# Kernel tuning notes

Measured on AMD Instinct MI355X. Metric: run time of the kernel, lower is better.

## Reference

```python
import jax, jax.numpy as jnp
import numpy as np

NUM_HEAD = 8
EMBED_DIM = 512


def setup_inputs() -> dict:
    key = jax.random.key(0)
    ks = jax.random.split(key, 9)
    B, N, D = 4, 2048, 512
    # xavier_uniform bound for square [D, D] weights
    bound = float(np.sqrt(6.0 / (D + EMBED_DIM)))
    return {
        "q": jax.random.normal(ks[0], (B, N, D), jnp.float32),
        "k": jax.random.normal(ks[1], (B, N, D), jnp.float32),
        "v": jax.random.normal(ks[2], (B, N, D), jnp.float32),
        "Wq": jax.random.uniform(ks[3], (D, EMBED_DIM), jnp.float32, -bound, bound),
        "Wk": jax.random.uniform(ks[4], (D, EMBED_DIM), jnp.float32, -bound, bound),
        "Wv": jax.random.uniform(ks[5], (D, EMBED_DIM), jnp.float32, -bound, bound),
        "bq": jnp.zeros((EMBED_DIM,), jnp.float32),
        "bk": jnp.zeros((EMBED_DIM,), jnp.float32),
        "bv": jnp.zeros((EMBED_DIM,), jnp.float32),
    }


def reference(q, k, v, Wq, Wk, Wv, bq, bk, bv):
    h = NUM_HEAD
    ch = EMBED_DIM // h
    B, N, _ = q.shape
    # linear projections
    Q = q @ Wq + bq  # [B, N, E]
    K = k @ Wk + bk
    V = v @ Wv + bv
    # split heads: b n (h ch) -> b h n ch
    Q = Q.reshape(B, N, h, ch).transpose(0, 2, 1, 3)
    K = K.reshape(B, N, h, ch).transpose(0, 2, 1, 3)
    V = V.reshape(B, N, h, ch).transpose(0, 2, 1, 3)
    scale = 1.0 / np.sqrt(ch).astype(np.float32)
    scores = jnp.einsum("bhqc,bhkc->bhqk", Q, K) * scale  # [B, h, N, N]
    attn = jax.nn.softmax(scores, axis=-1)
    out = jnp.einsum("bhqk,bhkc->bhqc", attn, V)  # [B, h, N, ch]
    # merge heads: b h n ch -> b n (h ch)
    return out.transpose(0, 2, 1, 3).reshape(B, N, EMBED_DIM)
```

## Files before the change

### kernel.cpp

```cpp
#include <hip/hip_runtime.h>
#include <hip/hip_bf16.h>
#include <cstdint>

#define B_ 4
#define N_ 2048
#define D_ 512
#define E_ 512
#define H_ 8
#define CH_ 64
#define M_ (B_*N_)

typedef __attribute__((ext_vector_type(8))) short bf16x8;
typedef __attribute__((ext_vector_type(4))) float f32x4;
typedef __attribute__((ext_vector_type(16))) float f32x16;
using u16 = unsigned short;
using u32 = unsigned int;

__device__ __forceinline__ u16 f2bf(float f) {
  union { __hip_bfloat16 h; u16 u; } cv;
  cv.h = __float2bfloat16(f);
  return cv.u;
}

__device__ __forceinline__ float fexp2(float x) {
#if __has_builtin(__builtin_amdgcn_exp2f)
  return __builtin_amdgcn_exp2f(x);
#else
  return exp2f(x);
#endif
}

__device__ __forceinline__ void async16(const void* g, void* l) {
  __builtin_amdgcn_global_load_lds(
      (__attribute__((address_space(1))) void*)(g),
      (__attribute__((address_space(3))) void*)(l),
      16, 0, 0);
}

__global__ void prep(const float* __restrict__ q, const float* __restrict__ k,
                     const float* __restrict__ v,
                     const float* __restrict__ Wq, const float* __restrict__ Wk,
                     const float* __restrict__ Wv,
                     u16* __restrict__ qb, u16* __restrict__ kb, u16* __restrict__ vb,
                     u16* __restrict__ tq, u16* __restrict__ tk, u16* __restrict__ tv) {
  int bid = blockIdx.x;
  if (bid < 12288) {
    int t = bid >> 12;
    const float* in = (t == 0) ? q : (t == 1 ? k : v);
    u16* outp = (t == 0) ? qb : (t == 1 ? kb : vb);
    int i = ((bid & 4095) << 8) + threadIdx.x;
    float4 f = reinterpret_cast<const float4*>(in)[i];
    ushort4 o;
    o.x = f2bf(f.x); o.y = f2bf(f.y); o.z = f2bf(f.z); o.w = f2bf(f.w);
    reinterpret_cast<ushort4*>(outp)[i] = o;
  } else {
    bid -= 12288;
    int t = bid >> 10;
    const float* W = (t == 0) ? Wq : (t == 1 ? Wk : Wv);
    u16* T = (t == 0) ? tq : (t == 1 ? tk : tv);
    int idx = ((bid & 1023) << 8) + threadIdx.x;
    int e = idx >> 9, kd = idx & 511;
    T[idx] = f2bf(W[kd * E_ + e]);
  }
}

#define GBM 128
#define GBN 128
#define GBK 64

__global__ __launch_bounds__(256) void proj_gemm(
    const u16* __restrict__ xq, const u16* __restrict__ xk, const u16* __restrict__ xv,
    const u16* __restrict__ wtq, const u16* __restrict__ wtk, const u16* __restrict__ wtv,
    const float* __restrict__ bq, const float* __restrict__ bk, const float* __restrict__ bv,
    u16* __restrict__ Qp, u16* __restrict__ Kp, u16* __restrict__ Vp) {
  const int z = blockIdx.z;
  const u16* X  = (z == 0) ? xq : (z == 1 ? xk : xv);
  const u16* WT = (z == 0) ? wtq : (z == 1 ? wtk : wtv);
  const float* bias = (z == 0) ? bq : (z == 1 ? bk : bv);
  u16* Out = (z == 0) ? Qp : (z == 1 ? Kp : Vp);
  const float scale = (z == 0) ? 0.18033688011112042f : 1.0f;
  const bool vlayout = (z == 2);

  __shared__ __align__(16) u16 As[GBM * GBK];
  __shared__ __align__(16) u16 Bs[GBN * GBK];

  const int tid = threadIdx.x;
  const int l = tid & 63, w = tid >> 6;
  const int wr = w >> 1, wc = w & 1;
  const int m0 = blockIdx.y * GBM;
  const int e0 = blockIdx.x * GBN;

  f32x4 acc[4][4] = {};

  for (int ks = 0; ks < D_ / GBK; ++ks) {
    const int k0 = ks * GBK;
#pragma unroll
    for (int i = 0; i < 4; ++i) {
      int o = i * 4096 + tid * 16;
      int row = o >> 7, colb = o & 127;
      int scol = colb ^ ((row & 7) << 4);
      async16((const char*)X  + ((size_t)(m0 + row) * D_ + k0) * 2 + scol, (char*)As + o);
      async16((const char*)WT + ((size_t)(e0 + row) * D_ + k0) * 2 + scol, (char*)Bs + o);
    }
    __syncthreads();
#pragma unroll
    for (int kk = 0; kk < 2; ++kk) {
      bf16x8 af[4], bfr[4];
#pragma unroll
      for (int m = 0; m < 4; ++m) {
        int row = wr * 64 + m * 16 + (l & 15);
        int addr = (row << 7) + kk * 64 + ((l >> 4) << 4);
        addr ^= (row & 7) << 4;
        af[m] = *reinterpret_cast<const bf16x8*>((const char*)As + addr);
      }
#pragma unroll
      for (int n = 0; n < 4; ++n) {
        int row = wc * 64 + n * 16 + (l & 15);
        int addr = (row << 7) + kk * 64 + ((l >> 4) << 4);
        addr ^= (row & 7) << 4;
        bfr[n] = *reinterpret_cast<const bf16x8*>((const char*)Bs + addr);
      }
#pragma unroll
      for (int m = 0; m < 4; ++m)
#pragma unroll
        for (int n = 0; n < 4; ++n)
          acc[m][n] = __builtin_amdgcn_mfma_f32_16x16x32_bf16(af[m], bfr[n], acc[m][n], 0, 0, 0);
    }
    __syncthreads();
  }

#pragma unroll
  for (int m = 0; m < 4; ++m) {
#pragma unroll
    for (int n = 0; n < 4; ++n) {
      int ge = e0 + wc * 64 + n * 16 + (l & 15);
      int h = ge >> 6, c = ge & 63;
      float bv_ = bias[ge];
      int gm0 = m0 + wr * 64 + m * 16 + ((l >> 4) << 2);
      int b = gm0 >> 11, nn0 = gm0 & 2047;
      if (vlayout) {
        short4 sv;
#pragma unroll
        for (int j = 0; j < 4; ++j)
          ((u16*)&sv)[j] = f2bf((acc[m][n][j] + bv_) * scale);
        int np = (((nn0 >> 2) ^ (nn0 >> 3)) & 1) ? (nn0 ^ 12) : nn0;
        *reinterpret_cast<short4*>(
            &Out[(((size_t)b * H_ + h) * CH_ + c) * N_ + np]) = sv;
      } else {
#pragma unroll
        for (int j = 0; j < 4; ++j) {
          u16 oval = f2bf((acc[m][n][j] + bv_) * scale);
          Out[((((size_t)b * H_ + h) * N_ + nn0 + j) << 6) + c] = oval;
        }
      }
    }
  }
}

#define QBLK 128
#define KVB 64
#define NTH 16

#define MFMA32(A, Bv, C) __builtin_amdgcn_mfma_f32_32x32x16_bf16((A), (Bv), (C), 0, 0, 0)

__global__ __launch_bounds__(512, 2) void attn_kernel(
    const u16* __restrict__ Qp, const u16* __restrict__ Kp, const u16* __restrict__ Vp,
    float* __restrict__ out) {
  __shared__ __align__(16) u16 Kb[2][2][KVB * 64];
  __shared__ __align__(16) u16 Vb[2][2][KVB * 64];

  const int tid = threadIdx.x;
  const int l = tid & 63, w = tid >> 6;
  const int wsub = w & 3, hf = w >> 2;
  const int qcol = l & 31, hi = l >> 5;

  const int beta = blockIdx.x;
  const int xcd = beta & 7, r = beta >> 3;
  const int bh = xcd * 4 + (r >> 4);
  const int qt = r & 15;

  const u16* Qh = Qp + (size_t)bh * N_ * CH_;
  const u16* Kh = Kp + (size_t)bh * N_ * CH_;
  const u16* Vh = Vp + (size_t)bh * CH_ * N_;
  const int bb = bh >> 3, hh = bh & 7;
  const int qrow = qt * QBLK + wsub * 32 + qcol;

  bf16x8 qf[4];
  {
    const u16* qptr = Qh + (size_t)qrow * CH_;
#pragma unroll
    for (int ks = 0; ks < 4; ++ks)
      qf[ks] = *reinterpret_cast<const bf16x8*>(qptr + ks * 16 + hi * 8);
  }

  f32x16 o0 = {}, o1 = {};
  float lrun = 0.f;

  const int rowA = qcol << 7;
  const int swz  = (l & 7) << 4;
  const int hi16 = hi << 4;
  const int st   = tid & 255;
  const int tb   = hf * NTH;

#define STAGE(BUF, KV) do {                                                      \
    _Pragma("unroll")                                                            \
    for (int i = 0; i < 2; ++i) {                                                \
      int o = i * 4096 + st * 16;                                                \
      int row = o >> 7, colb = o & 127;                                          \
      int scol = colb ^ ((row & 7) << 4);                                        \
      async16((const char*)Kh + ((size_t)((KV) + row) << 7) + scol,              \
              (char*)&Kb[BUF][hf][0] + o);                                       \
      async16((const char*)Vh + ((size_t)row * N_ + (KV)) * 2 + scol,            \
              (char*)&Vb[BUF][hf][0] + o);                                       \
    } } while (0)

#define TILE(BUF, TL) do {                                                       \
    if ((TL) + 1 < NTH) STAGE((BUF) ^ 1, (tb + (TL) + 1) * KVB);                 \
    f32x16 s0 = {}, s1 = {};                                                     \
    __builtin_amdgcn_s_setprio(1);                                               \
    _Pragma("unroll")                                                            \
    for (int ks = 0; ks < 4; ++ks) {                                             \
      int col = (ks * 32 + hi16) ^ swz;                                          \
      bf16x8 k0 = *reinterpret_cast<const bf16x8*>((const char*)&Kb[BUF][hf][0] + rowA + col);        \
      bf16x8 k1 = *reinterpret_cast<const bf16x8*>((const char*)&Kb[BUF][hf][0] + 4096 + rowA + col); \
      s0 = MFMA32(k0, qf[ks], s0);                                               \
      s1 = MFMA32(k1, qf[ks], s1);                                               \
    }                                                                            \
    __builtin_amdgcn_s_setprio(0);                                               \
    _Pragma("unroll")                                                            \
    for (int rr = 0; rr < 16; ++rr) { s0[rr] = fexp2(s0[rr]); s1[rr] = fexp2(s1[rr]); } \
    {                                                                            \
      float t0 = (s0[0] + s0[1]) + (s0[2] + s0[3]);                              \
      float t1 = (s0[4] + s0[5]) + (s0[6] + s0[7]);                              \
      float t2 = (s0[8] + s0[9]) + (s0[10] + s0[11]);                            \
      float t3 = (s0[12] + s0[13]) + (s0[14] + s0[15]);                          \
      float t4 = (s1[0] + s1[1]) + (s1[2] + s1[3]);                              \
      float t5 = (s1[4] + s1[5]) + (s1[6] + s1[7]);                              \
      float t6 = (s1[8] + s1[9]) + (s1[10] + s1[11]);                            \
      float t7 = (s1[12] + s1[13]) + (s1[14] + s1[15]);                          \
      float rsum = ((t0 + t1) + (t2 + t3)) + ((t4 + t5) + (t6 + t7));            \
      rsum += __shfl_xor(rsum, 32);                                              \
      lrun += rsum;                                                              \
    }                                                                            \
    __builtin_amdgcn_s_setprio(1);                                               \
    _Pragma("unroll")                                                            \
    for (int ks = 0; ks < 4; ++ks) {                                             \
      const f32x16& sv = (ks < 2) ? s0 : s1;                                     \
      const int b0 = 8 * (ks & 1);                                               \
      union { u16 us[8]; bf16x8 v8; } pu;                                        \
      _Pragma("unroll")                                                          \
      for (int j = 0; j < 8; ++j) pu.us[j] = f2bf(sv[b0 + j]);                   \
      int col = (ks * 32 + hi16) ^ swz;                                          \
      bf16x8 v0 = *reinterpret_cast<const bf16x8*>((const char*)&Vb[BUF][hf][0] + rowA + col);        \
      bf16x8 v1 = *reinterpret_cast<const bf16x8*>((const char*)&Vb[BUF][hf][0] + 4096 + rowA + col); \
      o0 = MFMA32(v0, pu.v8, o0);                                                \
      o1 = MFMA32(v1, pu.v8, o1);                                                \
    }                                                                            \
    __builtin_amdgcn_s_setprio(0);                                               \
    __syncthreads();                                                             \
  } while (0)

  STAGE(0, tb * KVB);
  __syncthreads();

  for (int tl = 0; tl < NTH; tl += 2) {
    TILE(0, tl);
    TILE(1, tl + 1);
  }

  float* shO = (float*)&Kb[0][0][0];
  float* shL = (float*)&Vb[0][0][0];
  if (hf == 1) {
    float* pb = shO + wsub * 2048 + l * 4;
#pragma unroll
    for (int c = 0; c < 4; ++c) {
      float4 s;
      s.x = o0[c * 4 + 0]; s.y = o0[c * 4 + 1];
      s.z = o0[c * 4 + 2]; s.w = o0[c * 4 + 3];
      *reinterpret_cast<float4*>(pb + c * 256) = s;
    }
#pragma unroll
    for (int c = 0; c < 4; ++c) {
      float4 s;
      s.x = o1[c * 4 + 0]; s.y = o1[c * 4 + 1];
      s.z = o1[c * 4 + 2]; s.w = o1[c * 4 + 3];
      *reinterpret_cast<float4*>(pb + (4 + c) * 256) = s;
    }
    shL[wsub * 64 + l] = lrun;
  }
  __syncthreads();
  if (hf == 0) {
    float inv = 1.0f / (lrun + shL[wsub * 64 + l]);
    const float* pb = shO + wsub * 2048 + l * 4;
    const size_t obase = ((size_t)bb * N_ + qrow) * E_ + hh * CH_;
#pragma unroll
    for (int c = 0; c < 4; ++c) {
      float4 p = *reinterpret_cast<const float4*>(pb + c * 256);
      float4 stv;
      stv.x = (o0[c * 4 + 0] + p.x) * inv;
      stv.y = (o0[c * 4 + 1] + p.y) * inv;
      stv.z = (o0[c * 4 + 2] + p.z) * inv;
      stv.w = (o0[c * 4 + 3] + p.w) * inv;
      *reinterpret_cast<float4*>(out + obase + 0 * 32 + c * 8 + hi * 4) = stv;
    }
#pragma unroll
    for (int c = 0; c < 4; ++c) {
      float4 p = *reinterpret_cast<const float4*>(pb + (4 + c) * 256);
      float4 stv;
      stv.x = (o1[c * 4 + 0] + p.x) * inv;
      stv.y = (o1[c * 4 + 1] + p.y) * inv;
      stv.z = (o1[c * 4 + 2] + p.z) * inv;
      stv.w = (o1[c * 4 + 3] + p.w) * inv;
      *reinterpret_cast<float4*>(out + obase + 1 * 32 + c * 8 + hi * 4) = stv;
    }
  }
#undef STAGE
#undef TILE
}

extern "C" void kernel_launch(void* const* d_in, const int* in_sizes, int n_in,
                              void* d_out, int out_size, void* d_ws, size_t ws_size,
                              hipStream_t stream) {
  const float* q  = (const float*)d_in[0];
  const float* k  = (const float*)d_in[1];
  const float* v  = (const float*)d_in[2];
  const float* Wq = (const float*)d_in[3];
  const float* Wk = (const float*)d_in[4];
  const float* Wv = (const float*)d_in[5];
  const float* bq = (const float*)d_in[6];
  const float* bk = (const float*)d_in[7];
  const float* bv = (const float*)d_in[8];
  float* out = (float*)d_out;

  u16* wtq = (u16*)d_ws;
  u16* wtk = wtq + (size_t)D_ * E_;
  u16* wtv = wtk + (size_t)D_ * E_;
  u16* Qp  = wtv + (size_t)D_ * E_;
  u16* Kp  = Qp + (size_t)M_ * E_;
  u16* Vp  = Kp + (size_t)M_ * E_;
  u16* qb  = Vp + (size_t)M_ * E_;
  u16* kb  = qb + (size_t)M_ * D_;
  u16* vb  = kb + (size_t)M_ * D_;

  prep<<<15360, 256, 0, stream>>>(q, k, v, Wq, Wk, Wv, qb, kb, vb, wtq, wtk, wtv);
  proj_gemm<<<dim3(E_ / GBN, M_ / GBM, 3), 256, 0, stream>>>(
      qb, kb, vb, wtq, wtk, wtv, bq, bk, bv, Qp, Kp, Vp);
  attn_kernel<<<512, 512, 0, stream>>>(Qp, Kp, Vp, out);
}
```

Baseline: 87.90 us.

## Halve attention KV tile to 32 keys with new LDS swizzle layouts

Shrinks the KV tile per pipeline step from 64 to 32 keys and doubles the number of tiles, so each wave issues one QK MFMA chain and two PV pairs per step. The K and V staging layouts and XOR swizzles are redesigned for the narrower tile, with one async copy per thread each, and the softmax-sum scratch moves to its own shared array. This cuts LDS use, which could raise occupancy, and reduces register pressure from the score accumulators. In exchange there are twice as many barriers and smaller MFMA batches between them, which may expose latency.

```diff
diff --git a/kernel.cpp b/kernel.cpp
--- a/kernel.cpp
+++ b/kernel.cpp
@@ -158,16 +158,17 @@
 }
 
 #define QBLK 128
-#define KVB 64
-#define NTH 16
+#define KVB 32
+#define NTH 32
 
 #define MFMA32(A, Bv, C) __builtin_amdgcn_mfma_f32_32x32x16_bf16((A), (Bv), (C), 0, 0, 0)
 
 __global__ __launch_bounds__(512, 2) void attn_kernel(
     const u16* __restrict__ Qp, const u16* __restrict__ Kp, const u16* __restrict__ Vp,
     float* __restrict__ out) {
-  __shared__ __align__(16) u16 Kb[2][2][KVB * 64];
-  __shared__ __align__(16) u16 Vb[2][2][KVB * 64];
+  __shared__ __align__(16) u16 Kb[2][2][2048];
+  __shared__ __align__(16) u16 Vb[2][2][2048];
+  __shared__ float shL[4][64];
 
   const int tid = threadIdx.x;
   const int l = tid & 63, w = tid >> 6;
@@ -196,63 +197,60 @@
   f32x16 o0 = {}, o1 = {};
   float lrun = 0.f;
 
-  const int rowA = qcol << 7;
-  const int swz  = (l & 7) << 4;
-  const int hi16 = hi << 4;
-  const int st   = tid & 255;
-  const int tb   = hf * NTH;
+  const int kbase = ((qcol >> 1) << 8) + ((qcol & 1) << 4);
+  const int kxor  = (qcol >> 1) & 7;
+  const int vbase = ((qcol >> 2) << 8) + ((qcol & 3) << 4);
+  const int vxor  = (qcol >> 2) & 3;
+
+  const int st = tid & 255;
+  const int tb = hf * (N_ / 2);
+
+  const int so    = st * 16;
+  const int kpair = so >> 8;
+  const int krow  = (kpair << 1) | ((so >> 4) & 1);
+  const int kcol  = ((((so >> 5) & 7) ^ (kpair & 7)) << 4) | (so & 15);
+  const int vquad = so >> 8;
+  const int vrow  = (vquad << 2) | ((so >> 4) & 3);
+  const int vcol  = ((((so >> 6) & 3) ^ (vquad & 3)) << 4) | (so & 15);
 
 #define STAGE(BUF, KV) do {                                                      \
-    _Pragma("unroll")                                                            \
-    for (int i = 0; i < 2; ++i) {                                                \
-      int o = i * 4096 + st * 16;                                                \
-      int row = o >> 7, colb = o & 127;                                          \
-      int scol = colb ^ ((row & 7) << 4);                                        \
-      async16((const char*)Kh + ((size_t)((KV) + row) << 7) + scol,              \
-              (char*)&Kb[BUF][hf][0] + o);                                       \
-      async16((const char*)Vh + ((size_t)row * N_ + (KV)) * 2 + scol,            \
-              (char*)&Vb[BUF][hf][0] + o);                                       \
-    } } while (0)
+    async16((const char*)Kh + (size_t)((KV) + krow) * 128 + kcol,                \
+            (char*)&Kb[BUF][hf][0] + so);                                        \
+    async16((const char*)Vh + (size_t)vrow * (N_ * 2) + (KV) * 2 + vcol,         \
+            (char*)&Vb[BUF][hf][0] + so);                                        \
+  } while (0)
 
 #define TILE(BUF, TL) do {                                                       \
-    if ((TL) + 1 < NTH) STAGE((BUF) ^ 1, (tb + (TL) + 1) * KVB);                 \
-    f32x16 s0 = {}, s1 = {};                                                     \
+    if ((TL) + 1 < NTH) STAGE((BUF) ^ 1, tb + ((TL) + 1) * KVB);                 \
+    f32x16 s0 = {};                                                              \
     __builtin_amdgcn_s_setprio(1);                                               \
     _Pragma("unroll")                                                            \
     for (int ks = 0; ks < 4; ++ks) {                                             \
-      int col = (ks * 32 + hi16) ^ swz;                                          \
-      bf16x8 k0 = *reinterpret_cast<const bf16x8*>((const char*)&Kb[BUF][hf][0] + rowA + col);        \
-      bf16x8 k1 = *reinterpret_cast<const bf16x8*>((const char*)&Kb[BUF][hf][0] + 4096 + rowA + col); \
-      s0 = MFMA32(k0, qf[ks], s0);                                               \
-      s1 = MFMA32(k1, qf[ks], s1);                                               \
+      int ka = kbase + ((((ks << 1) | hi) ^ kxor) << 5);                         \
+      bf16x8 kf = *reinterpret_cast<const bf16x8*>((const char*)&Kb[BUF][hf][0] + ka); \
+      s0 = MFMA32(kf, qf[ks], s0);                                               \
     }                                                                            \
     __builtin_amdgcn_s_setprio(0);                                               \
     _Pragma("unroll")                                                            \
-    for (int rr = 0; rr < 16; ++rr) { s0[rr] = fexp2(s0[rr]); s1[rr] = fexp2(s1[rr]); } \
+    for (int rr = 0; rr < 16; ++rr) s0[rr] = fexp2(s0[rr]);                      \
     {                                                                            \
       float t0 = (s0[0] + s0[1]) + (s0[2] + s0[3]);                              \
       float t1 = (s0[4] + s0[5]) + (s0[6] + s0[7]);                              \
       float t2 = (s0[8] + s0[9]) + (s0[10] + s0[11]);                            \
       float t3 = (s0[12] + s0[13]) + (s0[14] + s0[15]);                          \
-      float t4 = (s1[0] + s1[1]) + (s1[2] + s1[3]);                              \
-      float t5 = (s1[4] + s1[5]) + (s1[6] + s1[7]);                              \
-      float t6 = (s1[8] + s1[9]) + (s1[10] + s1[11]);                            \
-      float t7 = (s1[12] + s1[13]) + (s1[14] + s1[15]);                          \
-      float rsum = ((t0 + t1) + (t2 + t3)) + ((t4 + t5) + (t6 + t7));            \
+      float rsum = (t0 + t1) + (t2 + t3);                                        \
       rsum += __shfl_xor(rsum, 32);                                              \
       lrun += rsum;                                                              \
     }                                                                            \
     __builtin_amdgcn_s_setprio(1);                                               \
     _Pragma("unroll")                                                            \
-    for (int ks = 0; ks < 4; ++ks) {                                             \
-      const f32x16& sv = (ks < 2) ? s0 : s1;                                     \
-      const int b0 = 8 * (ks & 1);                                               \
+    for (int ks = 0; ks < 2; ++ks) {                                             \
       union { u16 us[8]; bf16x8 v8; } pu;                                        \
       _Pragma("unroll")                                                          \
-      for (int j = 0; j < 8; ++j) pu.us[j] = f2bf(sv[b0 + j]);                   \
-      int col = (ks * 32 + hi16) ^ swz;                                          \
-      bf16x8 v0 = *reinterpret_cast<const bf16x8*>((const char*)&Vb[BUF][hf][0] + rowA + col);        \
-      bf16x8 v1 = *reinterpret_cast<const bf16x8*>((const char*)&Vb[BUF][hf][0] + 4096 + rowA + col); \
+      for (int j = 0; j < 8; ++j) pu.us[j] = f2bf(s0[ks * 8 + j]);               \
+      int va = vbase + ((((ks << 1) | hi) ^ vxor) << 6);                         \
+      bf16x8 v0 = *reinterpret_cast<const bf16x8*>((const char*)&Vb[BUF][hf][0] + va);        \
+      bf16x8 v1 = *reinterpret_cast<const bf16x8*>((const char*)&Vb[BUF][hf][0] + va + 2048); \
       o0 = MFMA32(v0, pu.v8, o0);                                                \
       o1 = MFMA32(v1, pu.v8, o1);                                                \
     }                                                                            \
@@ -260,7 +258,7 @@
     __syncthreads();                                                             \
   } while (0)
 
-  STAGE(0, tb * KVB);
+  STAGE(0, tb);
   __syncthreads();
 
   for (int tl = 0; tl < NTH; tl += 2) {
@@ -268,10 +266,9 @@
     TILE(1, tl + 1);
   }
 
-  float* shO = (float*)&Kb[0][0][0];
-  float* shL = (float*)&Vb[0][0][0];
+  float* pb = (wsub < 2) ? ((float*)&Kb[0][0][0] + wsub * 2048 + l * 4)
+                         : ((float*)&Vb[0][0][0] + (wsub - 2) * 2048 + l * 4);
   if (hf == 1) {
-    float* pb = shO + wsub * 2048 + l * 4;
 #pragma unroll
     for (int c = 0; c < 4; ++c) {
       float4 s;
@@ -286,12 +283,11 @@
       s.z = o1[c * 4 + 2]; s.w = o1[c * 4 + 3];
       *reinterpret_cast<float4*>(pb + (4 + c) * 256) = s;
     }
-    shL[wsub * 64 + l] = lrun;
+    shL[wsub][l] = lrun;
   }
   __syncthreads();
   if (hf == 0) {
-    float inv = 1.0f / (lrun + shL[wsub * 64 + l]);
-    const float* pb = shO + wsub * 2048 + l * 4;
+    float inv = 1.0f / (lrun + shL[wsub][l]);
     const size_t obase = ((size_t)bb * N_ + qrow) * E_ + hh * CH_;
 #pragma unroll
     for (int c = 0; c < 4; ++c) {
@@ -301,7 +297,7 @@
       stv.y = (o0[c * 4 + 1] + p.y) * inv;
       stv.z = (o0[c * 4 + 2] + p.z) * inv;
       stv.w = (o0[c * 4 + 3] + p.w) * inv;
-      *reinterpret_cast<float4*>(out + obase + 0 * 32 + c * 8 + hi * 4) = stv;
+      *reinterpret_cast<float4*>(out + obase + c * 8 + hi * 4) = stv;
     }
 #pragma unroll
     for (int c = 0; c < 4; ++c) {
@@ -311,7 +307,7 @@
       stv.y = (o1[c * 4 + 1] + p.y) * inv;
       stv.z = (o1[c * 4 + 2] + p.z) * inv;
       stv.w = (o1[c * 4 + 3] + p.w) * inv;
-      *reinterpret_cast<float4*>(out + obase + 1 * 32 + c * 8 + hi * 4) = stv;
+      *reinterpret_cast<float4*>(out + obase + 32 + c * 8 + hi * 4) = stv;
     }
   }
 #undef STAGE
```

Result: no change. 86.36 us (-1.8%).
